# Kernel tuning notes

Hardware: AMD Instinct MI355X
Metric: run time of the kernel (lower is better)

The kernel has to match this reference:

```python
import jax, jax.numpy as jnp
import numpy as np

B, C, H, W = 8, 256, 160, 160

def setup_inputs() -> dict:
    key = jax.random.key(0)
    kx, kw, kh = jax.random.split(key, 3)
    x = jax.random.normal(kx, (B, C, H, W), dtype=jnp.float32)
    # kaiming_normal fan_in, relu -> std = sqrt(2/fan_in)
    fcw_w = jax.random.normal(kw, (1, W), dtype=jnp.float32) * np.float32(np.sqrt(2.0 / W))
    fch_w = jax.random.normal(kh, (1, H), dtype=jnp.float32) * np.float32(np.sqrt(2.0 / H))
    fcw_b = jnp.zeros((1,), dtype=jnp.float32)
    fch_b = jnp.zeros((1,), dtype=jnp.float32)
    return {"x": x, "fcw_w": fcw_w, "fcw_b": fcw_b, "fch_w": fch_w, "fch_b": fch_b}

def reference(x, fcw_w, fcw_b, fch_w, fch_b):
    b, c, h, w = x.shape
    xr = x.reshape(b * c, h, w)                                   # (n,h,w)
    # fc_w: Linear(w,1) then softmax over h (dim=1 of (n,h,1))
    alpha = jax.nn.softmax(jnp.einsum('nhw,w->nh', xr, fcw_w[0]) + fcw_b[0], axis=1)  # (n,h)
    # repeat+bmm == broadcasting a softmax-weighted row-sum to every row:
    # x_c[n,i,:] = sum_h alpha[n,h] * x[n,h,:]  (same for all i)
    row = jnp.einsum('nh,nhw->nw', alpha, xr)                      # (n,w)
    # fc_h on x_c^T (n,w,h): each h-column of x_c^T equals row, so the
    # Linear(h,1) reduces to row * sum(fch_w) + bias (identical math)
    beta = jax.nn.softmax(row * jnp.sum(fch_w[0]) + fch_b[0], axis=1)  # (n,w)
    # second repeat+bmm collapses to a scalar per (b,c): sum_w beta*row
    s = jnp.einsum('nw,nw->n', beta, row)                          # (n,)
    out = jnp.broadcast_to(s[:, None, None], (b * c, h, w)).reshape(b, c, h, w)
    return out
```

## Files before the change

kernel.cpp:

```cpp
#include <hip/hip_runtime.h>


#define HH 160
#define WW 160
#define NPLANE (HH * WW)
#define BLOCK 320
#define RPT 20
#define QN 40
#define PSTR 41

__global__ void __launch_bounds__(BLOCK) sa1_reduce(
    const float* __restrict__ x,
    const float* __restrict__ fcw_w,
    const float* __restrict__ fch_w,
    float* __restrict__ out)
{
    const int n = blockIdx.x;
    const int t = threadIdx.x;
    const int q = t % QN;
    const int v = t / QN;

    __shared__ float pbuf[HH * PSTR];
    __shared__ float larr[HH];
    __shared__ float sc[4];

    const float* xp = x + (size_t)n * NPLANE;

    const float4 ww = *(const float4*)(fcw_w + 4 * q);

    float4 xr[RPT];
#pragma unroll
    for (int r = 0; r < RPT; ++r)
        xr[r] = *(const float4*)(xp + (size_t)(v * RPT + r) * WW + 4 * q);

#pragma unroll
    for (int r = 0; r < RPT; ++r) {
        float p = xr[r].x * ww.x + xr[r].y * ww.y + xr[r].z * ww.z + xr[r].w * ww.w;
        pbuf[(v * RPT + r) * PSTR + q] = p;
    }
    __syncthreads();

    if (t < HH) {
        const float* pr = pbuf + t * PSTR;
        float s0 = 0.f, s1 = 0.f, s2 = 0.f, s3 = 0.f;
#pragma unroll
        for (int qq = 0; qq < QN; qq += 4) {
            s0 += pr[qq]; s1 += pr[qq + 1]; s2 += pr[qq + 2]; s3 += pr[qq + 3];
        }
        larr[t] = (s0 + s1) + (s2 + s3);
    }
    __syncthreads();

    if (t < 32) {
        float lv[5];
#pragma unroll
        for (int j = 0; j < 5; ++j) lv[j] = larr[t + 32 * j];
        float m = lv[0];
#pragma unroll
        for (int j = 1; j < 5; ++j) m = fmaxf(m, lv[j]);
#pragma unroll
        for (int off = 16; off >= 1; off >>= 1)
            m = fmaxf(m, __shfl_down(m, off, 32));
        m = __shfl(m, 0, 32);
        float z = 0.f;
#pragma unroll
        for (int j = 0; j < 5; ++j) z += __expf(lv[j] - m);
#pragma unroll
        for (int off = 16; off >= 1; off >>= 1)
            z += __shfl_down(z, off, 32);
        if (t == 0) { sc[0] = m; sc[1] = z; }
    } else if (t >= 64 && t < 96) {
        const int u = t - 64;
        float s = 0.f;
#pragma unroll
        for (int j = 0; j < 5; ++j) s += fch_w[u + 32 * j];
#pragma unroll
        for (int off = 16; off >= 1; off >>= 1)
            s += __shfl_down(s, off, 32);
        if (u == 0) sc[2] = s;
    }
    __syncthreads();

    const float m = sc[0];
    const float Z = sc[1];
    float4 rp = make_float4(0.f, 0.f, 0.f, 0.f);
#pragma unroll
    for (int r = 0; r < RPT; ++r) {
        float a = __expf(larr[v * RPT + r] - m);
        rp.x += a * xr[r].x; rp.y += a * xr[r].y;
        rp.z += a * xr[r].z; rp.w += a * xr[r].w;
    }
    __syncthreads();
    pbuf[v * WW + 4 * q + 0] = rp.x;
    pbuf[v * WW + 4 * q + 1] = rp.y;
    pbuf[v * WW + 4 * q + 2] = rp.z;
    pbuf[v * WW + 4 * q + 3] = rp.w;
    __syncthreads();

    if (t < WW) {
        float rs = 0.f;
#pragma unroll
        for (int vv = 0; vv < 8; ++vv) rs += pbuf[vv * WW + t];
        larr[t] = rs / Z;
    }
    __syncthreads();

    if (t < 32) {
        const float S = sc[2];
        float rv[5], bl[5];
#pragma unroll
        for (int j = 0; j < 5; ++j) { rv[j] = larr[t + 32 * j]; bl[j] = rv[j] * S; }
        float mb = bl[0];
#pragma unroll
        for (int j = 1; j < 5; ++j) mb = fmaxf(mb, bl[j]);
#pragma unroll
        for (int off = 16; off >= 1; off >>= 1)
            mb = fmaxf(mb, __shfl_down(mb, off, 32));
        mb = __shfl(mb, 0, 32);
        float zb = 0.f, sd = 0.f;
#pragma unroll
        for (int j = 0; j < 5; ++j) {
            float e = __expf(bl[j] - mb);
            zb += e; sd += e * rv[j];
        }
#pragma unroll
        for (int off = 16; off >= 1; off >>= 1) {
            zb += __shfl_down(zb, off, 32);
            sd += __shfl_down(sd, off, 32);
        }
        if (t == 0) out[(size_t)n * NPLANE] = sd / zb;
    }
}

__global__ void __launch_bounds__(256) sa1_bcast(float* __restrict__ out)
{
    const int n = blockIdx.x;
    const int t = threadIdx.x;
    float* op = out + (size_t)n * NPLANE;

    const float sv = op[0];
    __syncthreads();

    const float4 o = make_float4(sv, sv, sv, sv);
#pragma unroll
    for (int k = 0; k < 25; ++k)
        *(float4*)(op + 4 * (size_t)(k * 256 + t)) = o;
}

extern "C" void kernel_launch(void* const* d_in, const int* in_sizes, int n_in,
                              void* d_out, int out_size, void* d_ws, size_t ws_size,
                              hipStream_t stream) {
    const float* x     = (const float*)d_in[0];
    const float* fcw_w = (const float*)d_in[1];
    const float* fch_w = (const float*)d_in[3];
    float* out = (float*)d_out;

    const int nplanes = 8 * 256;
    sa1_reduce<<<nplanes, BLOCK, 0, stream>>>(x, fcw_w, fch_w, out);
    sa1_bcast<<<nplanes, 256, 0, stream>>>(out);
}
```

Measured before the change: 357.4 us.

## Split fused plane reduction into separate logits, attention and broadcast kernels

Replaces the single per-plane reduce kernel with three kernels. The first computes the per-row logits using one 64-lane wavefront per row and a shuffle reduction, writing them to workspace. The second reloads each plane column-wise to form the softmax-weighted row and the final scalar. The third broadcasts that scalar from workspace. The aim is to drop the large register and LDS footprint of the fused kernel and gain occupancy, at the cost of reading x twice and leaving 24 of 64 lanes idle in the logits pass.

```diff
diff --git a/kernel.cpp b/kernel.cpp
--- a/kernel.cpp
+++ b/kernel.cpp
@@ -4,143 +4,119 @@
 #define HH 160
 #define WW 160
 #define NPLANE (HH * WW)
-#define BLOCK 320
-#define RPT 20
-#define QN 40
-#define PSTR 41
+#define NPLANES 2048
+#define NROWS (NPLANES * HH)
 
-__global__ void __launch_bounds__(BLOCK) sa1_reduce(
+__global__ void __launch_bounds__(256) sa1_logits(
     const float* __restrict__ x,
     const float* __restrict__ fcw_w,
-    const float* __restrict__ fch_w,
-    float* __restrict__ out)
+    float* __restrict__ l)
 {
-    const int n = blockIdx.x;
-    const int t = threadIdx.x;
-    const int q = t % QN;
-    const int v = t / QN;
+    const int wid  = (blockIdx.x * 256 + threadIdx.x) >> 6;
+    const int lane = threadIdx.x & 63;
 
-    __shared__ float pbuf[HH * PSTR];
-    __shared__ float larr[HH];
-    __shared__ float sc[4];
+    float4 ww = make_float4(0.f, 0.f, 0.f, 0.f);
+    if (lane < 40) ww = *(const float4*)(fcw_w + 4 * lane);
 
-    const float* xp = x + (size_t)n * NPLANE;
-
-    const float4 ww = *(const float4*)(fcw_w + 4 * q);
-
-    float4 xr[RPT];
-#pragma unroll
-    for (int r = 0; r < RPT; ++r)
-        xr[r] = *(const float4*)(xp + (size_t)(v * RPT + r) * WW + 4 * q);
-
-#pragma unroll
-    for (int r = 0; r < RPT; ++r) {
-        float p = xr[r].x * ww.x + xr[r].y * ww.y + xr[r].z * ww.z + xr[r].w * ww.w;
-        pbuf[(v * RPT + r) * PSTR + q] = p;
-    }
-    __syncthreads();
-
-    if (t < HH) {
-        const float* pr = pbuf + t * PSTR;
-        float s0 = 0.f, s1 = 0.f, s2 = 0.f, s3 = 0.f;
-#pragma unroll
-        for (int qq = 0; qq < QN; qq += 4) {
-            s0 += pr[qq]; s1 += pr[qq + 1]; s2 += pr[qq + 2]; s3 += pr[qq + 3];
-        }
-        larr[t] = (s0 + s1) + (s2 + s3);
-    }
-    __syncthreads();
-
-    if (t < 32) {
-        float lv[5];
-#pragma unroll
-        for (int j = 0; j < 5; ++j) lv[j] = larr[t + 32 * j];
-        float m = lv[0];
-#pragma unroll
-        for (int j = 1; j < 5; ++j) m = fmaxf(m, lv[j]);
-#pragma unroll
-        for (int off = 16; off >= 1; off >>= 1)
-            m = fmaxf(m, __shfl_down(m, off, 32));
-        m = __shfl(m, 0, 32);
-        float z = 0.f;
-#pragma unroll
-        for (int j = 0; j < 5; ++j) z += __expf(lv[j] - m);
-#pragma unroll
-        for (int off = 16; off >= 1; off >>= 1)
-            z += __shfl_down(z, off, 32);
-        if (t == 0) { sc[0] = m; sc[1] = z; }
-    } else if (t >= 64 && t < 96) {
-        const int u = t - 64;
-        float s = 0.f;
-#pragma unroll
-        for (int j = 0; j < 5; ++j) s += fch_w[u + 32 * j];
-#pragma unroll
-        for (int off = 16; off >= 1; off >>= 1)
-            s += __shfl_down(s, off, 32);
-        if (u == 0) sc[2] = s;
-    }
-    __syncthreads();
-
-    const float m = sc[0];
-    const float Z = sc[1];
-    float4 rp = make_float4(0.f, 0.f, 0.f, 0.f);
-#pragma unroll
-    for (int r = 0; r < RPT; ++r) {
-        float a = __expf(larr[v * RPT + r] - m);
-        rp.x += a * xr[r].x; rp.y += a * xr[r].y;
-        rp.z += a * xr[r].z; rp.w += a * xr[r].w;
-    }
-    __syncthreads();
-    pbuf[v * WW + 4 * q + 0] = rp.x;
-    pbuf[v * WW + 4 * q + 1] = rp.y;
-    pbuf[v * WW + 4 * q + 2] = rp.z;
-    pbuf[v * WW + 4 * q + 3] = rp.w;
-    __syncthreads();
-
-    if (t < WW) {
-        float rs = 0.f;
-#pragma unroll
-        for (int vv = 0; vv < 8; ++vv) rs += pbuf[vv * WW + t];
-        larr[t] = rs / Z;
-    }
-    __syncthreads();
-
-    if (t < 32) {
-        const float S = sc[2];
-        float rv[5], bl[5];
-#pragma unroll
-        for (int j = 0; j < 5; ++j) { rv[j] = larr[t + 32 * j]; bl[j] = rv[j] * S; }
-        float mb = bl[0];
-#pragma unroll
-        for (int j = 1; j < 5; ++j) mb = fmaxf(mb, bl[j]);
-#pragma unroll
-        for (int off = 16; off >= 1; off >>= 1)
-            mb = fmaxf(mb, __shfl_down(mb, off, 32));
-        mb = __shfl(mb, 0, 32);
-        float zb = 0.f, sd = 0.f;
-#pragma unroll
-        for (int j = 0; j < 5; ++j) {
-            float e = __expf(bl[j] - mb);
-            zb += e; sd += e * rv[j];
+#pragma unroll 4
+    for (int k = 0; k < 40; ++k) {
+        const int r = wid + (k << 13);
+        float p = 0.f;
+        if (lane < 40) {
+            const float4 xv = *(const float4*)(x + (size_t)r * WW + 4 * lane);
+            p = xv.x * ww.x + xv.y * ww.y + xv.z * ww.z + xv.w * ww.w;
         }
 #pragma unroll
-        for (int off = 16; off >= 1; off >>= 1) {
-            zb += __shfl_down(zb, off, 32);
-            sd += __shfl_down(sd, off, 32);
-        }
-        if (t == 0) out[(size_t)n * NPLANE] = sd / zb;
+        for (int off = 32; off >= 1; off >>= 1)
+            p += __shfl_xor(p, off, 64);
+        if (lane == 0) l[r] = p;
     }
 }
 
-__global__ void __launch_bounds__(256) sa1_bcast(float* __restrict__ out)
+__global__ void __launch_bounds__(256) sa1_attn(
+    const float* __restrict__ x,
+    const float* __restrict__ fch_w,
+    const float* __restrict__ l,
+    float* __restrict__ s_out)
+{
+    const int n    = blockIdx.x;
+    const int t    = threadIdx.x;
+    const int lane = t & 63;
+    const int wv   = t >> 6;
+
+    __shared__ float albuf[HH];
+    __shared__ float pmax[4], psum[4], pS[4], pzb[4], psd[4];
+
+    float lv = -1e30f, fv = 0.f;
+    if (t < HH) { lv = l[n * HH + t]; fv = fch_w[t]; }
+    float m = lv, fs = fv;
+#pragma unroll
+    for (int off = 32; off >= 1; off >>= 1) {
+        m  = fmaxf(m, __shfl_xor(m, off, 64));
+        fs += __shfl_xor(fs, off, 64);
+    }
+    if (lane == 0) { pmax[wv] = m; pS[wv] = fs; }
+    __syncthreads();
+    m = fmaxf(fmaxf(pmax[0], pmax[1]), fmaxf(pmax[2], pmax[3]));
+    const float S = pS[0] + pS[1] + pS[2] + pS[3];
+
+    float e = 0.f;
+    if (t < HH) { e = __expf(lv - m); albuf[t] = e; }
+    float zs = e;
+#pragma unroll
+    for (int off = 32; off >= 1; off >>= 1)
+        zs += __shfl_xor(zs, off, 64);
+    if (lane == 0) psum[wv] = zs;
+    __syncthreads();
+    const float Z = psum[0] + psum[1] + psum[2] + psum[3];
+
+    float acc0 = 0.f, acc1 = 0.f, acc2 = 0.f, acc3 = 0.f;
+    if (t < WW) {
+        const float* xp = x + (size_t)n * NPLANE + t;
+#pragma unroll 4
+        for (int h = 0; h < HH; h += 4) {
+            acc0 += albuf[h + 0] * xp[(h + 0) * WW];
+            acc1 += albuf[h + 1] * xp[(h + 1) * WW];
+            acc2 += albuf[h + 2] * xp[(h + 2) * WW];
+            acc3 += albuf[h + 3] * xp[(h + 3) * WW];
+        }
+    }
+    const float row = ((acc0 + acc1) + (acc2 + acc3)) / Z;
+
+    float bl = (t < WW) ? row * S : -1e30f;
+    float mb = bl;
+#pragma unroll
+    for (int off = 32; off >= 1; off >>= 1)
+        mb = fmaxf(mb, __shfl_xor(mb, off, 64));
+    if (lane == 0) pmax[wv] = mb;
+    __syncthreads();
+    mb = fmaxf(fmaxf(pmax[0], pmax[1]), fmaxf(pmax[2], pmax[3]));
+
+    float e2 = (t < WW) ? __expf(bl - mb) : 0.f;
+    float zb = e2, sd = e2 * row;
+#pragma unroll
+    for (int off = 32; off >= 1; off >>= 1) {
+        zb += __shfl_xor(zb, off, 64);
+        sd += __shfl_xor(sd, off, 64);
+    }
+    if (lane == 0) { pzb[wv] = zb; psd[wv] = sd; }
+    __syncthreads();
+    if (t == 0) {
+        const float ZB = pzb[0] + pzb[1] + pzb[2] + pzb[3];
+        const float SD = psd[0] + psd[1] + psd[2] + psd[3];
+        s_out[n] = SD / ZB;
+    }
+}
+
+__global__ void __launch_bounds__(256) sa1_bcast(
+    const float* __restrict__ s_arr,
+    float* __restrict__ out)
 {
     const int n = blockIdx.x;
     const int t = threadIdx.x;
     float* op = out + (size_t)n * NPLANE;
 
-    const float sv = op[0];
-    __syncthreads();
-
+    const float sv = s_arr[n];
     const float4 o = make_float4(sv, sv, sv, sv);
 #pragma unroll
     for (int k = 0; k < 25; ++k)
@@ -155,7 +131,10 @@
     const float* fch_w = (const float*)d_in[3];
     float* out = (float*)d_out;
 
-    const int nplanes = 8 * 256;
-    sa1_reduce<<<nplanes, BLOCK, 0, stream>>>(x, fcw_w, fch_w, out);
-    sa1_bcast<<<nplanes, 256, 0, stream>>>(out);
+    float* l_ws = (float*)d_ws;
+    float* s_ws = l_ws + NROWS;
+
+    sa1_logits<<<NPLANES, 256, 0, stream>>>(x, fcw_w, l_ws);
+    sa1_attn  <<<NPLANES, 256, 0, stream>>>(x, fch_w, l_ws, s_ws);
+    sa1_bcast <<<NPLANES, 256, 0, stream>>>(s_ws, out);
 }
```

Measured after the change: 393.6 us. +10.2%, slower.
